# Optimization experiments

Hardware: AMD Instinct MI355X
Metric: run time of the kernel (lower is better)

## Reference

```python
import jax, jax.numpy as jnp
import numpy as np

B, L, D, H, S = 2, 2048, 1024, 16, 4
Dh = D // H
EPS = 1e-5


def setup_inputs() -> dict:
    key = jax.random.key(0)
    ks = jax.random.split(key, 12)
    sc = 0.02
    w = lambda k, shape: (jax.random.normal(k, shape, jnp.float32) * sc)
    M = 2 * S  # number of MHA blocks / dense linears
    inp = {
        "response": jax.random.normal(ks[0], (B, L, D), jnp.float32),
        "mask": jnp.broadcast_to(jnp.tril(jnp.ones((L, L), bool)), (B, L, L)),
        "Wq": w(ks[1], (M, D, D)), "bq": w(ks[2], (M, D)),
        "Wk": w(ks[3], (M, D, D)), "bk": w(ks[4], (M, D)),
        "Wv": w(ks[5], (M, D, D)), "bv": w(ks[6], (M, D)),
        "Wo": w(ks[7], (M, D, D)), "bo": w(ks[8], (M, D)),
        "Wd": w(ks[9], (M, D, D)), "bd": w(ks[10], (M, D)),
    }
    return inp


def _ln(x):
    # fresh LayerNorm(d) with default weight=1, bias=0, eps=1e-5
    m = jnp.mean(x, axis=-1, keepdims=True)
    v = jnp.mean((x - m) ** 2, axis=-1, keepdims=True)
    return (x - m) * jax.lax.rsqrt(v + EPS)


def _linear(x, W, b):
    # torch Linear: x @ W.T + b
    return jnp.einsum('bld,od->blo', x, W) + b


def _mha(x, i, mask, Wq, bq, Wk, bk, Wv, bv, Wo, bo):
    # self-attention: q = k = v = x
    split = lambda y: y.reshape(B, L, H, Dh).transpose(0, 2, 1, 3)  # (B,H,L,Dh)
    q = split(_linear(x, Wq[i], bq[i]))
    k = split(_linear(x, Wk[i], bk[i]))
    v = split(_linear(x, Wv[i], bv[i]))
    scores = jnp.einsum('bhqd,bhkd->bhqk', q, k) / jnp.sqrt(jnp.float32(Dh))
    if mask is not None:
        scores = jnp.where(mask[:, None, :, :], scores, -jnp.inf)
    p = jnp.nan_to_num(jax.nn.softmax(scores, axis=-1))
    o = jnp.einsum('bhqk,bhkd->bhqd', p, v).transpose(0, 2, 1, 3).reshape(B, L, D)
    return _linear(o, Wo[i], bo[i])


def reference(response, mask, Wq, bq, Wk, bk, Wv, bv, Wo, bo, Wd, bd):
    x = response
    for i in range(S):
        # masked self-attention + residual + LN
        x = _ln(x + _mha(x, 2 * i, mask, Wq, bq, Wk, bk, Wv, bv, Wo, bo))
        # encoder-attention sublayer (encMem is None -> unmasked self-attention)
        x = _ln(x + _mha(x, 2 * i + 1, None, Wq, bq, Wk, bk, Wv, bv, Wo, bo))
        # dense: linear[2i](LeakyReLU(linear[2i+1](x)))
        h = jax.nn.leaky_relu(_linear(x, Wd[2 * i + 1], bd[2 * i + 1]), negative_slope=0.01)
        h = _linear(h, Wd[2 * i], bd[2 * i])
        x = _ln(x + h)
    return x
```

## Files before the change

kernel.cpp:

```cpp
#include <hip/hip_runtime.h>
#include <stdint.h>
#include <stddef.h>

typedef __attribute__((ext_vector_type(8))) _Float16 f16x8;
typedef __attribute__((ext_vector_type(4))) _Float16 f16x4;
typedef __attribute__((ext_vector_type(4))) float    f32x4;

#define NB 2
#define NL 2048
#define ND 1024
#define NH 16
#define NROWS (NB*NL)

__device__ __forceinline__ void async16(void* lds, const void* g) {
  __builtin_amdgcn_global_load_lds(
      (const __attribute__((address_space(1))) void*)g,
      (__attribute__((address_space(3))) void*)lds, 16, 0, 0);
}

struct CvtArgs { const float* in[5]; _Float16* out[5]; };

__global__ __launch_bounds__(256) void cvt_all(CvtArgs a, int n16)
{
  const float* in  = a.in[blockIdx.z];
  _Float16*   out  = a.out[blockIdx.z];
  for (int i = blockIdx.x * blockDim.x + threadIdx.x; i < n16;
       i += gridDim.x * blockDim.x) {
    const f32x4* src = (const f32x4*)in + 4 * (size_t)i;
    f32x4 v0 = __builtin_nontemporal_load(src);
    f32x4 v1 = __builtin_nontemporal_load(src + 1);
    f32x4 v2 = __builtin_nontemporal_load(src + 2);
    f32x4 v3 = __builtin_nontemporal_load(src + 3);
    f16x8 o0 = {(_Float16)v0[0], (_Float16)v0[1], (_Float16)v0[2], (_Float16)v0[3],
                (_Float16)v1[0], (_Float16)v1[1], (_Float16)v1[2], (_Float16)v1[3]};
    f16x8 o1 = {(_Float16)v2[0], (_Float16)v2[1], (_Float16)v2[2], (_Float16)v2[3],
                (_Float16)v3[0], (_Float16)v3[1], (_Float16)v3[2], (_Float16)v3[3]};
    ((f16x8*)out)[2 * (size_t)i]     = o0;
    ((f16x8*)out)[2 * (size_t)i + 1] = o1;
  }
}

__global__ __launch_bounds__(256) void init_x(
    const float* __restrict__ r, _Float16* __restrict__ xh, int n8)
{
  for (int i = blockIdx.x * blockDim.x + threadIdx.x; i < n8;
       i += gridDim.x * blockDim.x) {
    float4 v0 = ((const float4*)r)[2 * i];
    float4 v1 = ((const float4*)r)[2 * i + 1];
    f16x8 o = {(_Float16)v0.x, (_Float16)v0.y, (_Float16)v0.z, (_Float16)v0.w,
               (_Float16)v1.x, (_Float16)v1.y, (_Float16)v1.z, (_Float16)v1.w};
    ((f16x8*)xh)[i] = o;
  }
}

struct GArgs {
  const _Float16* A;
  const _Float16* B[3];
  const float*    bias[3];
  void*           out[3];
  int             mode[3];
  int             ksplit;
};

__global__ __launch_bounds__(256, 4) void gemm_bt(GArgs ga)
{
  __shared__ _Float16 As[128 * 64];
  __shared__ _Float16 Bs[128 * 64];
  const int tid = threadIdx.x;
  const int w = tid >> 6, l = tid & 63;
  const int ql = l & 15, g = l >> 4;
  const int z = blockIdx.z;
  const int widx = ga.ksplit ? 0 : (blockIdx.x >> 3);
  const _Float16* Bw  = ga.B[widx];
  const float*   bias = ga.bias[widx];
  void*          outp = ga.ksplit ? ga.out[z] : ga.out[widx];
  const int      mode = ga.mode[widx];
  const int kbeg = ga.ksplit ? z * (ND / 2) : 0;
  const int kend = ga.ksplit ? kbeg + ND / 2 : ND;
  const bool dobias = (!ga.ksplit) || (z == 0);
  const int brow = blockIdx.y * 128;
  const int bcol = (blockIdx.x & 7) * 128;
  const int wm = w >> 1, wn = w & 1;
  f32x4 acc[4][4] = {};

  const int srow = w * 32 + (l >> 3);
  const int scol = ((l & 7) ^ (l >> 3)) << 3;
  const _Float16* Ag = ga.A + (size_t)(brow + srow) * ND + scol;
  const _Float16* Bg = Bw   + (size_t)(bcol + srow) * ND + scol;

  for (int k0 = kbeg; k0 < kend; k0 += 64) {
    {
      _Float16* AsW = &As[w * 2048];
      _Float16* BsW = &Bs[w * 2048];
#pragma unroll
      for (int i = 0; i < 4; ++i) {
        async16(AsW + i * 512, Ag + (size_t)i * 8 * ND + k0);
        async16(BsW + i * 512, Bg + (size_t)i * 8 * ND + k0);
      }
    }
    asm volatile("s_waitcnt vmcnt(0)" ::: "memory");
    __builtin_amdgcn_s_barrier();
    __builtin_amdgcn_s_setprio(1);
#pragma unroll
    for (int ks = 0; ks < 64; ks += 32) {
      const int cx = (ks + g * 8) ^ ((ql & 7) << 3);
      f16x8 af[4], bf[4];
#pragma unroll
      for (int mi = 0; mi < 4; ++mi)
        af[mi] = *(const f16x8*)&As[(wm * 64 + mi * 16 + ql) * 64 + cx];
#pragma unroll
      for (int nj = 0; nj < 4; ++nj)
        bf[nj] = *(const f16x8*)&Bs[(wn * 64 + nj * 16 + ql) * 64 + cx];
#pragma unroll
      for (int mi = 0; mi < 4; ++mi)
#pragma unroll
        for (int nj = 0; nj < 4; ++nj)
          acc[mi][nj] = __builtin_amdgcn_mfma_f32_16x16x32_f16(
              af[mi], bf[nj], acc[mi][nj], 0, 0, 0);
    }
    __builtin_amdgcn_s_setprio(0);
    asm volatile("s_waitcnt lgkmcnt(0)" ::: "memory");
    __builtin_amdgcn_s_barrier();
  }

  const int colb = bcol + wn * 64;
  const int rowb = brow + wm * 64 + g * 4;
  if (mode == 3) {
    _Float16* vt = (_Float16*)outp;
    const int bb = rowb >> 11;
#pragma unroll
    for (int nj = 0; nj < 4; ++nj) {
      const int col = colb + nj * 16 + ql;
      const float bv = bias[col];
      const int hh = col >> 6, d = col & 63;
      _Float16* vrow = vt + ((size_t)((bb * NH + hh) * 64 + d)) * NL;
#pragma unroll
      for (int mi = 0; mi < 4; ++mi) {
        const int krow = (rowb + mi * 16) & (NL - 1);
        f16x4 o;
#pragma unroll
        for (int r = 0; r < 4; ++r) o[r] = (_Float16)(acc[mi][nj][r] + bv);
        *(f16x4*)(vrow + krow) = o;
      }
    }
  } else {
    _Float16* oh = (_Float16*)outp;
#pragma unroll
    for (int nj = 0; nj < 4; ++nj) {
      const int col = colb + nj * 16 + ql;
      const float bv = dobias ? bias[col] : 0.f;
#pragma unroll
      for (int mi = 0; mi < 4; ++mi) {
#pragma unroll
        for (int r = 0; r < 4; ++r) {
          float v = acc[mi][nj][r] + bv;
          if (mode == 2) v = v > 0.f ? v : 0.01f * v;
          oh[(size_t)(rowb + mi * 16 + r) * ND + col] = (_Float16)v;
        }
      }
    }
  }
}

template<bool CAUSAL>
__global__ __launch_bounds__(512, 4) void attn_fwd(
    const _Float16* __restrict__ Q, const _Float16* __restrict__ K,
    const _Float16* __restrict__ Vt, _Float16* __restrict__ O)
{
  __shared__ _Float16 kv[3][2][64 * 64];
  __shared__ unsigned int pls[8][8 * 34];
  const int tid = threadIdx.x;
  const int w = tid >> 6, l = tid & 63;
  const int ql = l & 15, g = l >> 4;
  const int bi = blockIdx.x;
  const int within = bi >> 3;
  const int p = (bi & 7) + 8 * (within >> 4);
  const int h = p & 15, b = p >> 4;
  const int qt_raw = within & 15;
  const int qt = (CAUSAL && b) ? (NL / 128 - 1 - qt_raw) : qt_raw;
  const int qrow = qt * 128 + w * 16 + ql;

  const _Float16* Qp = Q + (size_t)(b * NL + qrow) * ND + h * 64 + g * 8;
  const f16x8 bq0 = *(const f16x8*)Qp;
  const f16x8 bq1 = *(const f16x8*)(Qp + 32);

  const int srow = w * 8 + (l >> 3);
  const int scol = ((l & 7) ^ (l >> 3)) << 3;
  const _Float16* Kg = K  + ((size_t)(b * NL) + srow) * ND + h * 64 + scol;
  const _Float16* Vg = Vt + ((size_t)((b * NH + h) * 64 + srow)) * NL + scol;

  const int msk  = (ql & 7) << 3;
  const int offA = ql * 64 + ((     g * 8) ^ msk);
  const int offB = ql * 64 + ((32 + g * 8) ^ msk);

  unsigned int* pw = &pls[w][0];
  f32x4 ot[4] = {};
  f32x4 sum_acc = {};
  const f16x8 ones = {(_Float16)1.f, (_Float16)1.f, (_Float16)1.f, (_Float16)1.f,
                      (_Float16)1.f, (_Float16)1.f, (_Float16)1.f, (_Float16)1.f};
  const int ntiles = CAUSAL ? (qt * 2 + 2) : (NL / 64);
  const float SCL = 0.125f * 1.44269504089f;
  const float M2  = 4.0f * 1.44269504089f;

  async16(&kv[0][0][w * 512], Kg);
  async16(&kv[0][1][w * 512], Vg);

  int cbuf = 0, sbuf = 1;
  for (int kt = 0; kt < ntiles; ++kt) {
    const size_t nk0 = (size_t)((kt + 1 < ntiles) ? kt + 1 : kt) * 64;
    async16(&kv[sbuf][0][w * 512], Kg + nk0 * ND);
    async16(&kv[sbuf][1][w * 512], Vg + nk0);
    asm volatile("s_waitcnt vmcnt(2)" ::: "memory");
    __builtin_amdgcn_s_barrier();

    const _Float16* kb = &kv[cbuf][0][0];
    const _Float16* vb = &kv[cbuf][1][0];
    const int k0 = kt * 64;
    f32x4 st[4] = {};
    __builtin_amdgcn_s_setprio(1);
#pragma unroll
    for (int sub = 0; sub < 4; ++sub) {
      const f16x8 a0 = *(const f16x8*)&kb[sub * 1024 + offA];
      const f16x8 a1 = *(const f16x8*)&kb[sub * 1024 + offB];
      st[sub] = __builtin_amdgcn_mfma_f32_16x16x32_f16(a0, bq0, st[sub], 0, 0, 0);
      st[sub] = __builtin_amdgcn_mfma_f32_16x16x32_f16(a1, bq1, st[sub], 0, 0, 0);
    }
    __builtin_amdgcn_s_setprio(0);
    float pv[16];
#pragma unroll
    for (int sub = 0; sub < 4; ++sub)
#pragma unroll
      for (int r = 0; r < 4; ++r) {
        float p2 = exp2f(__builtin_fmaf(st[sub][r], SCL, -M2));
        if (CAUSAL && (k0 + sub * 16 + g * 4 + r) > qrow) p2 = 0.f;
        pv[sub * 4 + r] = p2;
      }

#pragma unroll
    for (int sub = 0; sub < 2; ++sub) {
      uint2 uu;
      uu.x = __builtin_bit_cast(unsigned int,
                __builtin_amdgcn_cvt_pkrtz(pv[sub * 4 + 0], pv[sub * 4 + 1]));
      uu.y = __builtin_bit_cast(unsigned int,
                __builtin_amdgcn_cvt_pkrtz(pv[sub * 4 + 2], pv[sub * 4 + 3]));
      *(uint2*)&pw[(sub * 4 + g) * 34 + 2 * ql] = uu;
    }
    {
      uint2 lo = *(const uint2*)&pw[(2 * g    ) * 34 + 2 * ql];
      uint2 hi = *(const uint2*)&pw[(2 * g + 1) * 34 + 2 * ql];
      uint4 ui; ui.x = lo.x; ui.y = lo.y; ui.z = hi.x; ui.w = hi.y;
      const f16x8 pf = __builtin_bit_cast(f16x8, ui);
      __builtin_amdgcn_s_setprio(1);
#pragma unroll
      for (int dt = 0; dt < 4; ++dt) {
        const f16x8 vf = *(const f16x8*)&vb[dt * 1024 + offA];
        ot[dt] = __builtin_amdgcn_mfma_f32_16x16x32_f16(vf, pf, ot[dt], 0, 0, 0);
      }
      sum_acc = __builtin_amdgcn_mfma_f32_16x16x32_f16(ones, pf, sum_acc, 0, 0, 0);
      __builtin_amdgcn_s_setprio(0);
    }
#pragma unroll
    for (int sub = 2; sub < 4; ++sub) {
      uint2 uu;
      uu.x = __builtin_bit_cast(unsigned int,
                __builtin_amdgcn_cvt_pkrtz(pv[sub * 4 + 0], pv[sub * 4 + 1]));
      uu.y = __builtin_bit_cast(unsigned int,
                __builtin_amdgcn_cvt_pkrtz(pv[sub * 4 + 2], pv[sub * 4 + 3]));
      *(uint2*)&pw[((sub - 2) * 4 + g) * 34 + 2 * ql] = uu;
    }
    {
      uint2 lo = *(const uint2*)&pw[(2 * g    ) * 34 + 2 * ql];
      uint2 hi = *(const uint2*)&pw[(2 * g + 1) * 34 + 2 * ql];
      uint4 ui; ui.x = lo.x; ui.y = lo.y; ui.z = hi.x; ui.w = hi.y;
      const f16x8 pf = __builtin_bit_cast(f16x8, ui);
      __builtin_amdgcn_s_setprio(1);
#pragma unroll
      for (int dt = 0; dt < 4; ++dt) {
        const f16x8 vf = *(const f16x8*)&vb[dt * 1024 + offB];
        ot[dt] = __builtin_amdgcn_mfma_f32_16x16x32_f16(vf, pf, ot[dt], 0, 0, 0);
      }
      sum_acc = __builtin_amdgcn_mfma_f32_16x16x32_f16(ones, pf, sum_acc, 0, 0, 0);
      __builtin_amdgcn_s_setprio(0);
    }
    cbuf = sbuf;
    sbuf = sbuf + 1 == 3 ? 0 : sbuf + 1;
  }

  const float inv = 1.f / sum_acc[0];
#pragma unroll
  for (int dt = 0; dt < 4; ++dt) {
    f16x4 o;
#pragma unroll
    for (int r = 0; r < 4; ++r) o[r] = (_Float16)(ot[dt][r] * inv);
    *(f16x4*)(O + (size_t)(b * NL + qrow) * ND + h * 64 + dt * 16 + g * 4) = o;
  }
}

template<bool FINAL>
__global__ __launch_bounds__(256) void resid_ln(
    const _Float16* __restrict__ xh_in, const _Float16* __restrict__ d0,
    const _Float16* __restrict__ d1,
    _Float16* __restrict__ xh_out, float* __restrict__ xf)
{
  const int row = blockIdx.x, tid = threadIdx.x;
  const f16x4 xv = ((const f16x4*)(xh_in + (size_t)row * ND))[tid];
  const f16x4 v0 = ((const f16x4*)(d0 + (size_t)row * ND))[tid];
  const f16x4 v1 = ((const f16x4*)(d1 + (size_t)row * ND))[tid];
  const float a = (float)xv[0] + (float)v0[0] + (float)v1[0];
  const float b = (float)xv[1] + (float)v0[1] + (float)v1[1];
  const float c = (float)xv[2] + (float)v0[2] + (float)v1[2];
  const float d = (float)xv[3] + (float)v0[3] + (float)v1[3];
  float s = a + b + c + d;
  float ss = a * a + b * b + c * c + d * d;
#pragma unroll
  for (int m = 1; m < 64; m <<= 1) {
    s  += __shfl_xor(s, m);
    ss += __shfl_xor(ss, m);
  }
  __shared__ float red[8];
  if ((tid & 63) == 0) { red[tid >> 6] = s; red[4 + (tid >> 6)] = ss; }
  __syncthreads();
  const float S  = red[0] + red[1] + red[2] + red[3];
  const float SS = red[4] + red[5] + red[6] + red[7];
  const float mean = S * (1.0f / ND);
  const float var  = SS * (1.0f / ND) - mean * mean;
  const float rstd = rsqrtf(fmaxf(var, 0.f) + 1e-5f);
  const float ya = (a - mean) * rstd, yb = (b - mean) * rstd;
  const float yc = (c - mean) * rstd, yd = (d - mean) * rstd;
  if (FINAL) {
    float4 y; y.x = ya; y.y = yb; y.z = yc; y.w = yd;
    ((float4*)(xf + (size_t)row * ND))[tid] = y;
  } else {
    f16x4 yh = {(_Float16)ya, (_Float16)yb, (_Float16)yc, (_Float16)yd};
    ((f16x4*)(xh_out + (size_t)row * ND))[tid] = yh;
  }
}

extern "C" void kernel_launch(void* const* d_in, const int* in_sizes, int n_in,
                              void* d_out, int out_size, void* d_ws, size_t ws_size,
                              hipStream_t stream)
{
  (void)in_sizes; (void)n_in; (void)out_size; (void)ws_size;
  const float* response = (const float*)d_in[0];
  const float* Wq = (const float*)d_in[2];
  const float* bq = (const float*)d_in[3];
  const float* Wk = (const float*)d_in[4];
  const float* bk = (const float*)d_in[5];
  const float* Wv = (const float*)d_in[6];
  const float* bv = (const float*)d_in[7];
  const float* Wo = (const float*)d_in[8];
  const float* bo = (const float*)d_in[9];
  const float* Wd = (const float*)d_in[10];
  const float* bd = (const float*)d_in[11];
  float* xf = (float*)d_out;

  const size_t MB = 1024 * 1024;
  char* p = (char*)d_ws;
  _Float16* Wq_h = (_Float16*)(p + 0 * MB);
  _Float16* Wk_h = (_Float16*)(p + 16 * MB);
  _Float16* Wv_h = (_Float16*)(p + 32 * MB);
  _Float16* Wo_h = (_Float16*)(p + 48 * MB);
  _Float16* Wd_h = (_Float16*)(p + 64 * MB);
  _Float16* xh   = (_Float16*)(p + 80 * MB);
  _Float16* Qh   = (_Float16*)(p + 88 * MB);
  _Float16* Kh   = (_Float16*)(p + 96 * MB);
  _Float16* Vth  = (_Float16*)(p + 104 * MB);
  _Float16* Oh   = (_Float16*)(p + 112 * MB);
  _Float16* h1   = Qh;
  _Float16* t0   = (_Float16*)(p + 96 * MB);
  _Float16* t1   = (_Float16*)(p + 104 * MB);

  const int wn16 = 8 * 1024 * 1024 / 16;
  CvtArgs ca = { { Wq, Wk, Wv, Wo, Wd }, { Wq_h, Wk_h, Wv_h, Wo_h, Wd_h } };
  cvt_all<<<dim3(1024, 1, 5), 256, 0, stream>>>(ca, wn16);
  init_x<<<1024, 256, 0, stream>>>(response, xh, NROWS * ND / 8);

  const dim3 g3(24, NROWS / 128, 1);
  const dim3 gs(8, NROWS / 128, 2);
  const dim3 gf(8, NROWS / 128, 1);
  const dim3 agrid(NL / 128 * NH * NB);

  for (int i = 0; i < 4; ++i) {
    for (int sub = 0; sub < 2; ++sub) {
      const int m = 2 * i + sub;
      const size_t wo = (size_t)m * MB;
      const size_t bf = (size_t)m * 1024;
      GArgs qkv = { xh,
                    { Wq_h + wo, Wk_h + wo, Wv_h + wo },
                    { bq + bf, bk + bf, bv + bf },
                    { Qh, Kh, Vth }, { 0, 0, 3 }, 0 };
      gemm_bt<<<g3, 256, 0, stream>>>(qkv);
      if (sub == 0) attn_fwd<true ><<<agrid, 512, 0, stream>>>(Qh, Kh, Vth, Oh);
      else          attn_fwd<false><<<agrid, 512, 0, stream>>>(Qh, Kh, Vth, Oh);
      GArgs oprj = { Oh,
                     { Wo_h + wo, nullptr, nullptr },
                     { bo + bf, nullptr, nullptr },
                     { t0, t1, nullptr }, { 0, 0, 0 }, 1 };
      gemm_bt<<<gs, 256, 0, stream>>>(oprj);
      resid_ln<false><<<NROWS, 256, 0, stream>>>(xh, t0, t1, xh, nullptr);
    }
    const size_t w1 = (size_t)(2 * i + 1) * MB, b1 = (size_t)(2 * i + 1) * 1024;
    const size_t w0 = (size_t)(2 * i) * MB,     b0 = (size_t)(2 * i) * 1024;
    GArgs f1 = { xh,
                 { Wd_h + w1, nullptr, nullptr },
                 { bd + b1, nullptr, nullptr },
                 { h1, nullptr, nullptr }, { 2, 0, 0 }, 0 };
    gemm_bt<<<gf, 256, 0, stream>>>(f1);
    GArgs f2 = { h1,
                 { Wd_h + w0, nullptr, nullptr },
                 { bd + b0, nullptr, nullptr },
                 { t0, t1, nullptr }, { 0, 0, 0 }, 1 };
    gemm_bt<<<gs, 256, 0, stream>>>(f2);
    if (i == 3) resid_ln<true ><<<NROWS, 256, 0, stream>>>(xh, t0, t1, nullptr, xf);
    else        resid_ln<false><<<NROWS, 256, 0, stream>>>(xh, t0, t1, xh, nullptr);
  }
}
```

Measured before the change: 1.170 ms.

## Merge input conversion into one launch and restructure attention buffering and masking

```diff
diff --git a/kernel.cpp b/kernel.cpp
--- a/kernel.cpp
+++ b/kernel.cpp
@@ -18,13 +18,14 @@
       (__attribute__((address_space(3))) void*)lds, 16, 0, 0);
 }
 
-struct CvtArgs { const float* in[5]; _Float16* out[5]; };
-
-__global__ __launch_bounds__(256) void cvt_all(CvtArgs a, int n16)
+struct CvtArgs { const float* in[6]; _Float16* out[6]; };
+
+__global__ __launch_bounds__(256) void cvt_all(CvtArgs a, int n16, int rn16)
 {
   const float* in  = a.in[blockIdx.z];
   _Float16*   out  = a.out[blockIdx.z];
-  for (int i = blockIdx.x * blockDim.x + threadIdx.x; i < n16;
+  const int n = (blockIdx.z == 5) ? rn16 : n16;
+  for (int i = blockIdx.x * blockDim.x + threadIdx.x; i < n;
        i += gridDim.x * blockDim.x) {
     const f32x4* src = (const f32x4*)in + 4 * (size_t)i;
     f32x4 v0 = __builtin_nontemporal_load(src);
@@ -35,21 +36,8 @@
                 (_Float16)v1[0], (_Float16)v1[1], (_Float16)v1[2], (_Float16)v1[3]};
     f16x8 o1 = {(_Float16)v2[0], (_Float16)v2[1], (_Float16)v2[2], (_Float16)v2[3],
                 (_Float16)v3[0], (_Float16)v3[1], (_Float16)v3[2], (_Float16)v3[3]};
-    ((f16x8*)out)[2 * (size_t)i]     = o0;
-    ((f16x8*)out)[2 * (size_t)i + 1] = o1;
-  }
-}
-
-__global__ __launch_bounds__(256) void init_x(
-    const float* __restrict__ r, _Float16* __restrict__ xh, int n8)
-{
-  for (int i = blockIdx.x * blockDim.x + threadIdx.x; i < n8;
-       i += gridDim.x * blockDim.x) {
-    float4 v0 = ((const float4*)r)[2 * i];
-    float4 v1 = ((const float4*)r)[2 * i + 1];
-    f16x8 o = {(_Float16)v0.x, (_Float16)v0.y, (_Float16)v0.z, (_Float16)v0.w,
-               (_Float16)v1.x, (_Float16)v1.y, (_Float16)v1.z, (_Float16)v1.w};
-    ((f16x8*)xh)[i] = o;
+    __builtin_nontemporal_store(o0, (f16x8*)out + 2 * (size_t)i);
+    __builtin_nontemporal_store(o1, (f16x8*)out + 2 * (size_t)i + 1);
   }
 }
 
@@ -163,12 +151,12 @@
 }
 
 template<bool CAUSAL>
-__global__ __launch_bounds__(512, 4) void attn_fwd(
+__global__ __launch_bounds__(512) void attn_fwd(
     const _Float16* __restrict__ Q, const _Float16* __restrict__ K,
     const _Float16* __restrict__ Vt, _Float16* __restrict__ O)
 {
-  __shared__ _Float16 kv[3][2][64 * 64];
-  __shared__ unsigned int pls[8][8 * 34];
+  __shared__ _Float16 kv[2][2][64 * 64];
+  __shared__ unsigned int pls[8][16 * 34];
   const int tid = threadIdx.x;
   const int w = tid >> 6, l = tid & 63;
   const int ql = l & 15, g = l >> 4;
@@ -179,6 +167,7 @@
   const int qt_raw = within & 15;
   const int qt = (CAUSAL && b) ? (NL / 128 - 1 - qt_raw) : qt_raw;
   const int qrow = qt * 128 + w * 16 + ql;
+  const int qmin = qt * 128 + w * 16;
 
   const _Float16* Qp = Q + (size_t)(b * NL + qrow) * ND + h * 64 + g * 8;
   const f16x8 bq0 = *(const f16x8*)Qp;
@@ -205,11 +194,11 @@
   async16(&kv[0][0][w * 512], Kg);
   async16(&kv[0][1][w * 512], Vg);
 
-  int cbuf = 0, sbuf = 1;
+  int cbuf = 0;
   for (int kt = 0; kt < ntiles; ++kt) {
     const size_t nk0 = (size_t)((kt + 1 < ntiles) ? kt + 1 : kt) * 64;
-    async16(&kv[sbuf][0][w * 512], Kg + nk0 * ND);
-    async16(&kv[sbuf][1][w * 512], Vg + nk0);
+    async16(&kv[cbuf ^ 1][0][w * 512], Kg + nk0 * ND);
+    async16(&kv[cbuf ^ 1][1][w * 512], Vg + nk0);
     asm volatile("s_waitcnt vmcnt(2)" ::: "memory");
     __builtin_amdgcn_s_barrier();
 
@@ -227,17 +216,25 @@
     }
     __builtin_amdgcn_s_setprio(0);
     float pv[16];
-#pragma unroll
-    for (int sub = 0; sub < 4; ++sub)
-#pragma unroll
-      for (int r = 0; r < 4; ++r) {
-        float p2 = exp2f(__builtin_fmaf(st[sub][r], SCL, -M2));
-        if (CAUSAL && (k0 + sub * 16 + g * 4 + r) > qrow) p2 = 0.f;
-        pv[sub * 4 + r] = p2;
-      }
-
-#pragma unroll
-    for (int sub = 0; sub < 2; ++sub) {
+    if (!CAUSAL || (k0 + 63 <= qmin)) {
+#pragma unroll
+      for (int sub = 0; sub < 4; ++sub)
+#pragma unroll
+        for (int r = 0; r < 4; ++r)
+          pv[sub * 4 + r] = exp2f(__builtin_fmaf(st[sub][r], SCL, -M2));
+    } else {
+#pragma unroll
+      for (int sub = 0; sub < 4; ++sub)
+#pragma unroll
+        for (int r = 0; r < 4; ++r) {
+          float p2 = exp2f(__builtin_fmaf(st[sub][r], SCL, -M2));
+          if ((k0 + sub * 16 + g * 4 + r) > qrow) p2 = 0.f;
+          pv[sub * 4 + r] = p2;
+        }
+    }
+
+#pragma unroll
+    for (int sub = 0; sub < 4; ++sub) {
       uint2 uu;
       uu.x = __builtin_bit_cast(unsigned int,
                 __builtin_amdgcn_cvt_pkrtz(pv[sub * 4 + 0], pv[sub * 4 + 1]));
@@ -245,45 +242,25 @@
                 __builtin_amdgcn_cvt_pkrtz(pv[sub * 4 + 2], pv[sub * 4 + 3]));
       *(uint2*)&pw[(sub * 4 + g) * 34 + 2 * ql] = uu;
     }
-    {
-      uint2 lo = *(const uint2*)&pw[(2 * g    ) * 34 + 2 * ql];
-      uint2 hi = *(const uint2*)&pw[(2 * g + 1) * 34 + 2 * ql];
+#pragma unroll
+    for (int hh = 0; hh < 2; ++hh) {
+      uint2 lo = *(const uint2*)&pw[(hh * 8 + 2 * g    ) * 34 + 2 * ql];
+      uint2 hi = *(const uint2*)&pw[(hh * 8 + 2 * g + 1) * 34 + 2 * ql];
       uint4 ui; ui.x = lo.x; ui.y = lo.y; ui.z = hi.x; ui.w = hi.y;
       const f16x8 pf = __builtin_bit_cast(f16x8, ui);
+      const int voff = hh ? offB : offA;
       __builtin_amdgcn_s_setprio(1);
 #pragma unroll
       for (int dt = 0; dt < 4; ++dt) {
-        const f16x8 vf = *(const f16x8*)&vb[dt * 1024 + offA];
+        const f16x8 vf = *(const f16x8*)&vb[dt * 1024 + voff];
         ot[dt] = __builtin_amdgcn_mfma_f32_16x16x32_f16(vf, pf, ot[dt], 0, 0, 0);
       }
       sum_acc = __builtin_amdgcn_mfma_f32_16x16x32_f16(ones, pf, sum_acc, 0, 0, 0);
       __builtin_amdgcn_s_setprio(0);
     }
-#pragma unroll
-    for (int sub = 2; sub < 4; ++sub) {
-      uint2 uu;
-      uu.x = __builtin_bit_cast(unsigned int,
-                __builtin_amdgcn_cvt_pkrtz(pv[sub * 4 + 0], pv[sub * 4 + 1]));
-      uu.y = __builtin_bit_cast(unsigned int,
-                __builtin_amdgcn_cvt_pkrtz(pv[sub * 4 + 2], pv[sub * 4 + 3]));
-      *(uint2*)&pw[((sub - 2) * 4 + g) * 34 + 2 * ql] = uu;
-    }
-    {
-      uint2 lo = *(const uint2*)&pw[(2 * g    ) * 34 + 2 * ql];
-      uint2 hi = *(const uint2*)&pw[(2 * g + 1) * 34 + 2 * ql];
-      uint4 ui; ui.x = lo.x; ui.y = lo.y; ui.z = hi.x; ui.w = hi.y;
-      const f16x8 pf = __builtin_bit_cast(f16x8, ui);
-      __builtin_amdgcn_s_setprio(1);
-#pragma unroll
-      for (int dt = 0; dt < 4; ++dt) {
-        const f16x8 vf = *(const f16x8*)&vb[dt * 1024 + offB];
-        ot[dt] = __builtin_amdgcn_mfma_f32_16x16x32_f16(vf, pf, ot[dt], 0, 0, 0);
-      }
-      sum_acc = __builtin_amdgcn_mfma_f32_16x16x32_f16(ones, pf, sum_acc, 0, 0, 0);
-      __builtin_amdgcn_s_setprio(0);
-    }
-    cbuf = sbuf;
-    sbuf = sbuf + 1 == 3 ? 0 : sbuf + 1;
+    asm volatile("s_waitcnt lgkmcnt(0)" ::: "memory");
+    __builtin_amdgcn_s_barrier();
+    cbuf ^= 1;
   }
 
   const float inv = 1.f / sum_acc[0];
@@ -371,9 +348,10 @@
   _Float16* t1   = (_Float16*)(p + 104 * MB);
 
   const int wn16 = 8 * 1024 * 1024 / 16;
-  CvtArgs ca = { { Wq, Wk, Wv, Wo, Wd }, { Wq_h, Wk_h, Wv_h, Wo_h, Wd_h } };
-  cvt_all<<<dim3(1024, 1, 5), 256, 0, stream>>>(ca, wn16);
-  init_x<<<1024, 256, 0, stream>>>(response, xh, NROWS * ND / 8);
+  const int rn16 = NROWS * ND / 16;
+  CvtArgs ca = { { Wq, Wk, Wv, Wo, Wd, response },
+                 { Wq_h, Wk_h, Wv_h, Wo_h, Wd_h, xh } };
+  cvt_all<<<dim3(1024, 1, 6), 256, 0, stream>>>(ca, wn16, rn16);
 
   const dim3 g3(24, NROWS / 128, 1);
   const dim3 gs(8, NROWS / 128, 2);
```

Measured after the change: 1.230 ms. 1.05x slower.
